# Performance work log

Hardware: AMD Instinct MI355X
Metric: run time of the kernel (lower is better)

The kernel has to match this reference:

```python
import jax, jax.numpy as jnp
import numpy as np

GAMMA = 0.9          # EMA momentum for prototype update
N_CLASSES = 201      # 200 classes + 1 background
K_PROTO = 5          # prototypes per class
FG_THRESH = 0.5      # pca_fg_threshold
SK_EPS = 0.05        # sinkhorn temperature (SwAV-style)
SK_ITERS = 3         # sinkhorn iterations
PCA_ITERS = 10       # niter of torch.pca_lowrank


def _l2norm(x, axis=-1):
    return x / jnp.maximum(jnp.linalg.norm(x, axis=axis, keepdims=True), 1e-12)


def _pca_first_component(X, key):
    # Randomized power iteration for the top left singular vector of the
    # centered data (mirrors torch.pca_lowrank(X, q=1, center=True, niter=10)).
    Xc = X - X.mean(0, keepdims=True)            # [N, D]
    G = Xc.T @ Xc                                # [D, D]
    v = jax.random.normal(key, (X.shape[1],), X.dtype)
    v = v / jnp.linalg.norm(v)
    def body(v, _):
        v = G @ v
        return v / jnp.maximum(jnp.linalg.norm(v), 1e-12), None
    v, _ = jax.lax.scan(body, v, None, length=PCA_ITERS)
    u = Xc @ v                                   # [N]
    return u / jnp.maximum(jnp.linalg.norm(u), 1e-12)


def _masked_sinkhorn(logits, mask):
    # logits: [C, BN, K], mask: [C, BN] bool (rows belonging to class c).
    # Vectorized equivalent of the per-class sinkhorn_knopp(L_c): returns a
    # row-stochastic assignment on the masked rows, balanced over the K cols.
    tiny = 1e-9
    m = mask[..., None].astype(logits.dtype)     # [C, BN, 1]
    Q = jnp.exp(logits / SK_EPS) * m
    n_c = jnp.maximum(mask.sum(-1).astype(logits.dtype), 1.0)[:, None, None]
    K = Q.shape[-1]
    Q = Q / jnp.maximum(Q.sum((-2, -1), keepdims=True), tiny)
    for _ in range(SK_ITERS):
        Q = Q / jnp.maximum(Q.sum(-2, keepdims=True), tiny) / K   # balance cols
        Q = Q * m
        Q = Q / jnp.maximum(Q.sum(-1, keepdims=True), tiny) / n_c # balance rows
        Q = Q * m
    return Q * n_c  # each masked row sums to 1


def setup_inputs() -> dict:
    key = jax.random.key(0)
    k1, k2, k3 = jax.random.split(key, 3)
    B, n_patches, dim = 32, 1024, 768
    patch_tokens = jax.random.normal(k1, (B, n_patches, dim), jnp.float32)
    prototypes = 0.02 * jax.random.normal(k2, (N_CLASSES, K_PROTO, dim), jnp.float32)
    labels = jax.random.randint(k3, (B,), 0, 200).astype(jnp.int64)
    return {"patch_tokens": patch_tokens, "prototypes": prototypes, "labels": labels}


def reference(patch_tokens, prototypes, labels):
    B, n_patches, D = patch_tokens.shape

    pt_norm = _l2norm(patch_tokens)              # [B, N, D]
    proto_norm = _l2norm(prototypes)             # [C, K, D]
    # B n_patches dim, C K dim -> B n_patches C K
    logits = jnp.einsum('bnd,ckd->bnck', pt_norm, proto_norm)

    # ---- get_pseudo_patch_labels (PCA foreground extraction) ----
    X = patch_tokens.reshape(-1, D)
    U = _pca_first_component(X, jax.random.key(1))
    U_scaled = (U - U.min()) / (U.max() - U.min())
    fg = (U_scaled < FG_THRESH).reshape(B, n_patches)
    patch_labels = jnp.where(fg, labels[:, None], N_CLASSES - 1)  # [B, N] int

    # ---- update_prototypes, vectorized over the 201-class python loop ----
    pl_flat = patch_labels.reshape(-1)                            # [B*N]
    L = jnp.transpose(logits.reshape(-1, N_CLASSES, K_PROTO), (1, 0, 2))  # [C, BN, K]
    class_ids = jnp.arange(N_CLASSES)
    mask = pl_flat[None, :] == class_ids[:, None]                 # [C, BN]
    Q = _masked_sinkhorn(L, mask)                                 # [C, BN, K]
    # P_c_new = L_c_assignment.T @ I_c, batched over classes
    P_new = jnp.einsum('cnk,nd->ckd', Q, pt_norm.reshape(-1, D))  # [C, K, D]
    present = (labels[None, :] == class_ids[:, None]).any(-1)     # 'c in labels'
    ema = GAMMA * prototypes + (1.0 - GAMMA) * P_new              # momentum_update
    new_prototypes = jnp.where(present[:, None, None], ema, prototypes)

    image_prototype_logits = logits.max(1)        # [B, C, K]
    class_logits = image_prototype_logits.sum(-1) # [B, C]
    return class_logits, image_prototype_logits, new_prototypes
```

## Files before the change

### kernel.cpp

```cpp
#include <hip/hip_runtime.h>
#include <stdint.h>
#include <stddef.h>

#define DEV static __device__ __forceinline__

typedef __attribute__((ext_vector_type(8))) short bf16x8;
typedef __attribute__((ext_vector_type(4))) float f32x4;
typedef __attribute__((ext_vector_type(4))) int i32x4;

DEV float bf2f(unsigned short u){ union{unsigned int i; float f;} v; v.i = ((unsigned int)u)<<16; return v.f; }
DEV unsigned short f2bf(float f){ union{float f; unsigned int i;} v; v.f=f; unsigned int i=v.i;
  return (unsigned short)((i + 0x7FFFu + ((i>>16)&1u)) >> 16); }
DEV unsigned int fenc(float x){ unsigned int i = __float_as_uint(x); return (i & 0x80000000u) ? ~i : (i | 0x80000000u); }
DEV float fdec(unsigned int e){ unsigned int i = (e & 0x80000000u) ? (e & 0x7FFFFFFFu) : ~e; return __uint_as_float(i); }

DEV float waveSum(float s){
  for (int m=32;m;m>>=1) s += __shfl_xor(s, m, 64);
  return s;
}

DEV float blockSum(float v, float* red){
  int t = threadIdx.x;
  red[t] = v; __syncthreads();
  for (int k=128;k>0;k>>=1){ if (t<k) red[t] += red[t+k]; __syncthreads(); }
  float r = red[0]; __syncthreads();
  return r;
}

DEV void gl16(const void* g, void* lds){
  __builtin_amdgcn_global_load_lds(
      (const __attribute__((address_space(1))) void*)g,
      (__attribute__((address_space(3))) void*)lds, 16, 0, 0);
}

DEV float erfinv_f(float x){
  float w = -log1pf(-__fmul_rn(x,x));
  float p;
  if (w < 5.0f){
    w = w - 2.5f;
    p = 2.81022636e-08f;
    p = 3.43273939e-07f + p*w;
    p = -3.5233877e-06f + p*w;
    p = -4.39150654e-06f + p*w;
    p = 0.00021858087f + p*w;
    p = -0.00125372503f + p*w;
    p = -0.00417768164f + p*w;
    p = 0.246640727f + p*w;
    p = 1.50140941f + p*w;
  } else {
    w = sqrtf(w) - 3.0f;
    p = -0.000200214257f;
    p = 0.000100950558f + p*w;
    p = 0.00134934322f + p*w;
    p = -0.00367342844f + p*w;
    p = 0.00573950773f + p*w;
    p = -0.0076224613f + p*w;
    p = 0.00943887047f + p*w;
    p = 1.00167406f + p*w;
    p = 2.83297682f + p*w;
  }
  return p*x;
}

#define BN_TOT 32768
#define DIM 768
#define NCLS 201
#define KP 5
#define CKPAD 1024
#define GSPLIT 32
#define PSPLIT 8


__global__ void k_setup(unsigned int* ipl_enc, int* cnt, int* cur, int* present,
                        unsigned int* minmax, float* meansum,
                        const int* __restrict__ raw, int* __restrict__ lab,
                        float* __restrict__ v,
                        const float* __restrict__ protos, unsigned short* __restrict__ protn){
  int i = blockIdx.x*256 + threadIdx.x;
  ipl_enc[i] = 0u;
  if (i < NCLS){ cnt[i]=0; cur[i]=0; present[i]=0; }
  if (i < DIM) meansum[i] = 0.f;
  if (i == 0){
    minmax[0]=0xFFFFFFFFu; minmax[1]=0u;
    bool is64 = true;
    for (int j=0;j<8;j++){
      int lo = raw[2*j], hi = raw[2*j+1];
      if (hi != 0 || lo < 0 || lo >= NCLS-1){ is64 = false; break; }
    }
    for (int j=0;j<32;j++) lab[j] = is64 ? raw[2*j] : raw[j];
  }
  if (i < DIM){
    unsigned int ks[3] = {0u, 1u, 0x1BD11BDBu};
    const int rot0[4] = {13,15,26,6};
    const int rot1[4] = {17,29,16,24};
    unsigned int x0 = 0u, x1 = (unsigned int)i;
    x0 += ks[0]; x1 += ks[1];
    #pragma unroll
    for (int g=0; g<5; g++){
      const int* rr = (g&1) ? rot1 : rot0;
      #pragma unroll
      for (int j=0;j<4;j++){
        x0 += x1;
        x1 = (x1 << rr[j]) | (x1 >> (32-rr[j]));
        x1 ^= x0;
      }
      x0 += ks[(g+1)%3];
      x1 += ks[(g+2)%3] + (unsigned int)(g+1);
    }
    unsigned int b = x0 ^ x1;
    const float lo = __uint_as_float(0xBF7FFFFFu);
    const float sq2 = __uint_as_float(0x3FB504F3u);
    float f = __uint_as_float((b>>9) | 0x3F800000u) - 1.0f;
    float uu = __fadd_rn(__fmul_rn(f, 2.0f), lo);
    uu = fmaxf(lo, uu);
    v[i] = sq2 * erfinv_f(uu);
  }
  int l = threadIdx.x & 63;
  #pragma unroll
  for (int rr=0; rr<2; rr++){
    int row = blockIdx.x*8 + (threadIdx.x>>6)*2 + rr;
    if (row >= NCLS*KP){
      for (int j=0;j<12;j++) protn[(size_t)row*DIM + l + j*64] = 0;
    } else {
      const float* p = protos + (size_t)row*DIM;
      float x[12]; float s = 0.f;
      for (int j=0;j<12;j++){ x[j] = p[l + j*64]; s += x[j]*x[j]; }
      s = waveSum(s);
      float inv = 1.0f / fmaxf(sqrtf(s), 1e-12f);
      for (int j=0;j<12;j++) protn[(size_t)row*DIM + l + j*64] = f2bf(x[j]*inv);
    }
  }
}

__global__ void k_trans(const float* __restrict__ X, signed char* __restrict__ q1T,
                        signed char* __restrict__ q2T, float* __restrict__ meansum){
  __shared__ float tile[64][65];
  __shared__ float colsum[4][64];
  int n0 = blockIdx.x*64, c0 = blockIdx.y*64;
  int t = threadIdx.x;
  float part = 0.f;
  for (int i=0;i<16;i++){
    int idx = t + i*256; int r = idx>>6, c = idx&63;
    float x = X[(size_t)(n0+r)*DIM + c0+c];
    tile[r][c] = x;
    part += x;
  }
  colsum[t>>6][t&63] = part;
  __syncthreads();
  for (int i=0;i<4;i++){
    int flat = t + i*256;
    int c = flat>>4;
    int ng = flat&15;
    unsigned int p1 = 0, p2 = 0;
    #pragma unroll
    for (int j=0;j<4;j++){
      float x = tile[ng*4+j][c];
      int q1 = (int)rintf(x*16.0f);
      q1 = max(-127, min(127, q1));
      float r2 = x - (float)q1*(1.0f/16.0f);
      int q2 = (int)rintf(r2*2048.0f);
      q2 = max(-127, min(127, q2));
      p1 |= ((unsigned int)(q1 & 0xff)) << (8*j);
      p2 |= ((unsigned int)(q2 & 0xff)) << (8*j);
    }
    size_t o = (size_t)(c0+c)*BN_TOT + n0 + ng*4;
    *(unsigned int*)&q1T[o] = p1;
    *(unsigned int*)&q2T[o] = p2;
  }
  if (t < 64){
    float s = colsum[0][t]+colsum[1][t]+colsum[2][t]+colsum[3][t];
    atomicAdd(&meansum[c0+t], s);
  }
}

__global__ void k_ptn(const float* __restrict__ X, unsigned short* __restrict__ ptn){
  int row = blockIdx.x*4 + (threadIdx.x>>6);
  int l = threadIdx.x & 63;
  const float4* xr = (const float4*)(X + (size_t)row*DIM);
  float4 x4[3]; float s = 0.f;
  #pragma unroll
  for (int j=0;j<3;j++){
    x4[j] = xr[l + j*64];
    s += x4[j].x*x4[j].x + x4[j].y*x4[j].y + x4[j].z*x4[j].z + x4[j].w*x4[j].w;
  }
  s = waveSum(s);
  float inv = 1.0f / fmaxf(sqrtf(s), 1e-12f);
  #pragma unroll
  for (int j=0;j<3;j++){
    ushort4 o;
    o.x = f2bf(x4[j].x*inv); o.y = f2bf(x4[j].y*inv);
    o.z = f2bf(x4[j].z*inv); o.w = f2bf(x4[j].w*inv);
    *(ushort4*)&ptn[(size_t)row*DIM + 4*(l + j*64)] = o;
  }
}

__global__ __launch_bounds__(256) void k_gemm_logits(const unsigned short* __restrict__ A,
                                                     const unsigned short* __restrict__ Bt,
                                                     unsigned int* __restrict__ ipl_enc){
  __shared__ __align__(16) unsigned short As[128*32];
  __shared__ __align__(16) unsigned short Bs[128*32];
  __shared__ float red[2][2][64];
  int flat = blockIdx.y*8 + blockIdx.x;
  int xcd = flat & 7, j = flat >> 3;
  int mb = xcd*32 + (j>>3);
  int nb = j & 7;
  int t = threadIdx.x;
  int w = t>>6, l = t&63;
  int wr = w>>1, wc = w&1;

  int gu = (l&3) ^ ((l>>2)&3) ^ (l>>4);
  size_t lane_off = (size_t)(l>>2)*DIM + (size_t)gu*8;
  size_t baseA = (size_t)(mb*128)*DIM;
  size_t baseB = (size_t)(nb*128)*DIM;

  int physc = (l>>4) ^ (l&3) ^ ((l>>2)&3);
  int rdA = (wr*64 + (l&15))*32 + physc*8;
  int rdB = (wc*64 + (l&15))*32 + physc*8;

  f32x4 acc[4][4];
  #pragma unroll
  for (int m=0;m<4;m++)
    #pragma unroll
    for (int n=0;n<4;n++){ acc[m][n][0]=0.f; acc[m][n][1]=0.f; acc[m][n][2]=0.f; acc[m][n][3]=0.f; }

  for (int kt=0; kt<24; kt++){
    size_t k0 = (size_t)kt*32;
    __syncthreads();
    #pragma unroll
    for (int ci=0; ci<2; ci++){
      int c = w + ci*4;
      size_t roff = (size_t)(c*16)*DIM + k0 + lane_off;
      gl16(A + baseA + roff, &As[c*512]);
      gl16(Bt + baseB + roff, &Bs[c*512]);
    }
    __syncthreads();
    bf16x8 a[4], b[4];
    #pragma unroll
    for (int m=0;m<4;m++) a[m] = *(const bf16x8*)&As[rdA + m*512];
    #pragma unroll
    for (int n=0;n<4;n++) b[n] = *(const bf16x8*)&Bs[rdB + n*512];
    #pragma unroll
    for (int m=0;m<4;m++)
      #pragma unroll
      for (int n=0;n<4;n++)
        acc[m][n] = __builtin_amdgcn_mfma_f32_16x16x32_bf16(a[m], b[n], acc[m][n], 0,0,0);
  }
  float vmax[4];
  #pragma unroll
  for (int n=0;n<4;n++){
    float v = -1e30f;
    #pragma unroll
    for (int m=0;m<4;m++)
      #pragma unroll
      for (int r=0;r<4;r++) v = fmaxf(v, acc[m][n][r]);
    v = fmaxf(v, __shfl_xor(v, 16, 64));
    v = fmaxf(v, __shfl_xor(v, 32, 64));
    vmax[n] = v;
  }
  __syncthreads();
  if (l < 16){
    #pragma unroll
    for (int n=0;n<4;n++) red[wc][wr][n*16 + l] = vmax[n];
  }
  __syncthreads();
  if (t < 128){
    int wcc = t>>6, col = t&63;
    float v = fmaxf(red[wcc][0][col], red[wcc][1][col]);
    int gcol = nb*128 + wcc*64 + col;
    if (gcol < NCLS*KP){
      int b = (mb*128) >> 10;
      atomicMax(&ipl_enc[b*CKPAD + gcol], fenc(v));
    }
  }
}

__global__ __launch_bounds__(256) void k_gemm_G(const signed char* __restrict__ q1T,
                                                const signed char* __restrict__ q2T,
                                                float* __restrict__ Gpart){
  __shared__ __align__(16) signed char A1[128*64];
  __shared__ __align__(16) signed char A2[128*64];
  __shared__ __align__(16) signed char B1[128*64];
  __shared__ __align__(16) signed char B2[128*64];
  int b = blockIdx.x;
  int xcd = b & 7, q = b >> 3;
  int s = xcd + 8*(q/21);
  int p = q % 21;
  int ib = 0, rem = p;
  while (rem >= 6 - ib){ rem -= 6 - ib; ib++; }
  int jb = ib + rem;
  int t = threadIdx.x, w = t>>6, l = t&63;
  int wr = w>>1, wc = w&1;

  int gu = (l&3) ^ ((l>>2)&3) ^ (l>>4);
  size_t lane_off = (size_t)(l>>2)*BN_TOT + (size_t)gu*16;
  size_t baseA = (size_t)(ib*128)*BN_TOT;
  size_t baseB = (size_t)(jb*128)*BN_TOT;

  int physc = (l>>4) ^ (l&3) ^ ((l>>2)&3);
  int rdA = (wr*64 + (l&15))*64 + physc*16;
  int rdB = (wc*64 + (l&15))*64 + physc*16;

  i32x4 acc1[4][4], acc2[4][4];
  #pragma unroll
  for (int m=0;m<4;m++)
    #pragma unroll
    for (int n=0;n<4;n++){
      acc1[m][n][0]=0; acc1[m][n][1]=0; acc1[m][n][2]=0; acc1[m][n][3]=0;
      acc2[m][n][0]=0; acc2[m][n][1]=0; acc2[m][n][2]=0; acc2[m][n][3]=0;
    }

  for (int kt=0; kt<16; kt++){
    size_t k0 = (size_t)s*1024 + (size_t)kt*64;
    __syncthreads();
    #pragma unroll
    for (int ci=0; ci<2; ci++){
      int c = w + ci*4;
      size_t roff = (size_t)(c*16)*BN_TOT + k0 + lane_off;
      gl16(q1T + baseA + roff, &A1[c*1024]);
      gl16(q2T + baseA + roff, &A2[c*1024]);
      gl16(q1T + baseB + roff, &B1[c*1024]);
      gl16(q2T + baseB + roff, &B2[c*1024]);
    }
    __syncthreads();
    i32x4 b1[4], b2[4];
    #pragma unroll
    for (int n=0;n<4;n++){
      b1[n] = *(const i32x4*)&B1[rdB + n*1024];
      b2[n] = *(const i32x4*)&B2[rdB + n*1024];
    }
    #pragma unroll
    for (int m=0;m<4;m++){
      i32x4 a1 = *(const i32x4*)&A1[rdA + m*1024];
      i32x4 a2 = *(const i32x4*)&A2[rdA + m*1024];
      #pragma unroll
      for (int n=0;n<4;n++){
        acc1[m][n] = __builtin_amdgcn_mfma_i32_16x16x64_i8(a1, b1[n], acc1[m][n], 0,0,0);
        acc2[m][n] = __builtin_amdgcn_mfma_i32_16x16x64_i8(a1, b2[n], acc2[m][n], 0,0,0);
        acc2[m][n] = __builtin_amdgcn_mfma_i32_16x16x64_i8(a2, b1[n], acc2[m][n], 0,0,0);
      }
    }
  }

  const float S11 = 1.0f/256.0f;
  const float S12 = 1.0f/32768.0f;
  float* out = Gpart + (size_t)s*DIM*DIM;
  #pragma unroll
  for (int m=0;m<4;m++)
    #pragma unroll
    for (int n=0;n<4;n++)
      #pragma unroll
      for (int r=0;r<4;r++){
        int row = ib*128 + wr*64 + m*16 + (l>>4)*4 + r;
        int col = jb*128 + wc*64 + n*16 + (l&15);
        float val = (float)acc1[m][n][r]*S11 + (float)acc2[m][n][r]*S12;
        out[(size_t)row*DIM + col] = val;
        if (ib != jb) out[(size_t)col*DIM + row] = val;
      }
}

__global__ void k_gfix(const float* __restrict__ Gpart, const float* __restrict__ meansum,
                       float* __restrict__ G){
  int i4 = blockIdx.x*256 + threadIdx.x;
  int i = i4*4;
  int r = i/DIM, c = i%DIM;
  float4 s = make_float4(0.f,0.f,0.f,0.f);
  for (int p=0;p<GSPLIT;p++){
    float4 g = *(const float4*)&Gpart[(size_t)p*DIM*DIM + i];
    s.x += g.x; s.y += g.y; s.z += g.z; s.w += g.w;
  }
  const float invN = 1.0f/32768.0f;
  float mr = meansum[r]*invN;
  float4 mc = *(const float4*)&meansum[c];
  float4 o;
  o.x = s.x*invN - mr*mc.x*invN;
  o.y = s.y*invN - mr*mc.y*invN;
  o.z = s.z*invN - mr*mc.z*invN;
  o.w = s.w*invN - mr*mc.w*invN;
  *(float4*)&G[i] = o;
}

__global__ void k_mv(const float* __restrict__ G, const float* __restrict__ vin,
                     float* __restrict__ vout){
  __shared__ float vs[DIM];
  int t = threadIdx.x;
  for (int i=t;i<DIM;i+=256) vs[i] = vin[i];
  __syncthreads();
  int row = blockIdx.x*4 + (t>>6), l = t&63;
  const float* g = G + (size_t)row*DIM;
  float s = 0.f;
  for (int j=0;j<12;j++) s += g[l + j*64]*vs[l + j*64];
  s = waveSum(s);
  if (l==0) vout[row] = s;
}

__global__ void k_u(const float* __restrict__ X, const float* __restrict__ v,
                    const float* __restrict__ meansum,
                    float* __restrict__ u, unsigned int* __restrict__ minmax){
  __shared__ float vs[DIM];
  __shared__ float red[256];
  __shared__ float smn[4], smx[4];
  int t = threadIdx.x;
  for (int i=t;i<DIM;i+=256) vs[i] = v[i];
  __syncthreads();
  float ps = 0.f;
  for (int i=t;i<DIM;i+=256) ps += meansum[i]*(1.0f/32768.0f)*vs[i];
  float scal = blockSum(ps, red);
  int w = t>>6, l = t&63;
  float mn = 1e30f, mx = -1e30f;
  #pragma unroll
  for (int rr=0; rr<4; rr++){
    int row = blockIdx.x*16 + w*4 + rr;
    const float4* xr = (const float4*)(X + (size_t)row*DIM);
    float s = 0.f;
    #pragma unroll
    for (int j=0;j<3;j++){
      float4 x4 = xr[l + j*64];
      int base = 4*(l + j*64);
      s += x4.x*vs[base] + x4.y*vs[base+1] + x4.z*vs[base+2] + x4.w*vs[base+3];
    }
    s = waveSum(s);
    if (l==0){
      float val = s - scal;
      u[row] = val;
      mn = fminf(mn, val); mx = fmaxf(mx, val);
    }
  }
  if (l==0){ smn[w]=mn; smx[w]=mx; }
  __syncthreads();
  if (t==0){
    for (int k=1;k<4;k++){ mn = fminf(mn, smn[k]); mx = fmaxf(mx, smx[k]); }
    atomicMin(&minmax[0], fenc(mn));
    atomicMax(&minmax[1], fenc(mx));
  }
}

__global__ void k_pl(const float* __restrict__ u, const int* __restrict__ labels,
                     const unsigned int* __restrict__ minmax, int* __restrict__ pl,
                     int* __restrict__ cnt){
  int n = blockIdx.x*256 + threadIdx.x;
  float umin = fdec(minmax[0]), umax = fdec(minmax[1]);
  float us = (u[n]-umin)/(umax-umin);
  int c = (us < 0.5f) ? labels[n>>10] : (NCLS-1);
  pl[n] = c;
  if (c < NCLS-1) atomicAdd(&cnt[c], 1);
}

__global__ void k_offs(const int* __restrict__ cnt, int* __restrict__ offs,
                       const int* __restrict__ labels, int* __restrict__ present){
  if (threadIdx.x == 0){
    int acc = 0;
    for (int c=0;c<NCLS-1;c++){ offs[c] = acc; acc += cnt[c]; }
    offs[NCLS-1] = acc;
  }
  if (threadIdx.x < 32) atomicOr(&present[labels[threadIdx.x]], 1);
}

__global__ void k_scatter(const int* __restrict__ pl, const int* __restrict__ offs,
                          int* __restrict__ cur, int* __restrict__ idx){
  int n = blockIdx.x*256 + threadIdx.x;
  int c = pl[n];
  if (c < NCLS-1){
    int p = offs[c] + atomicAdd(&cur[c], 1);
    idx[p] = n;
  }
}

__global__ void k_qlog(const int* __restrict__ idx, const int* __restrict__ offs,
                       const int* __restrict__ pl, const unsigned short* __restrict__ ptn,
                       const unsigned short* __restrict__ protn, float* __restrict__ q){
  int i = blockIdx.x*4 + (threadIdx.x>>6);
  int l = threadIdx.x & 63;
  int total = offs[NCLS-1];
  if (i >= total) return;
  int n = idx[i];
  int c = pl[n];
  const unsigned short* pr = ptn + (size_t)n*DIM;
  float x[12];
  for (int j=0;j<12;j++) x[j] = bf2f(pr[l + j*64]);
  for (int k=0;k<KP;k++){
    const unsigned short* wv = protn + (size_t)(c*KP + k)*DIM;
    float s = 0.f;
    for (int j=0;j<12;j++) s += x[j]*bf2f(wv[l + j*64]);
    s = waveSum(s);
    if (l==0) q[(size_t)i*KP + k] = expf(s*20.0f);
  }
}

__global__ void k_sink(const int* __restrict__ cnt, const int* __restrict__ offs,
                       float* __restrict__ q){
  __shared__ float red[256];
  __shared__ float colf[KP];
  int c = blockIdx.x;
  int nc = cnt[c];
  if (nc == 0) return;
  int n0 = offs[c];
  float* Q = q + (size_t)n0*KP;
  int t = threadIdx.x;
  int tot5 = nc*KP;
  float s = 0.f;
  for (int i=t;i<tot5;i+=256) s += Q[i];
  float total = blockSum(s, red);
  float sc = 1.0f/fmaxf(total, 1e-9f);
  for (int i=t;i<tot5;i+=256) Q[i] *= sc;
  __syncthreads();
  float ncf = (float)nc;
  for (int it=0; it<3; it++){
    float cs[KP] = {0,0,0,0,0};
    for (int i=t;i<nc;i+=256){
      const float* row = Q + (size_t)i*KP;
      #pragma unroll
      for (int k=0;k<KP;k++) cs[k] += row[k];
    }
    for (int k=0;k<KP;k++){
      float v = blockSum(cs[k], red);
      if (t==0) colf[k] = 1.0f/(fmaxf(v,1e-9f)*(float)KP);
    }
    __syncthreads();
    for (int i=t;i<nc;i+=256){
      float* row = Q + (size_t)i*KP;
      float qq[KP]; float rs = 0.f;
      #pragma unroll
      for (int k=0;k<KP;k++){ qq[k] = row[k]*colf[k]; rs += qq[k]; }
      float rf = 1.0f/(fmaxf(rs,1e-9f)*ncf);
      #pragma unroll
      for (int k=0;k<KP;k++) row[k] = qq[k]*rf;
    }
    __syncthreads();
  }
  for (int i=t;i<tot5;i+=256) Q[i] *= ncf;
}

__global__ void k_pnew(const int* __restrict__ cnt, const int* __restrict__ offs,
                       const int* __restrict__ present, const int* __restrict__ idx,
                       const float* __restrict__ q, const unsigned short* __restrict__ ptn,
                       float* __restrict__ P4){
  int c = blockIdx.y, s = blockIdx.x;
  if (!present[c]) return;
  int nc = cnt[c], n0 = offs[c];
  int r0 = n0 + (nc*s)/PSPLIT;
  int r1 = n0 + (nc*(s+1))/PSPLIT;
  int t = threadIdx.x;
  float acc[KP][3];
  #pragma unroll
  for (int k=0;k<KP;k++){ acc[k][0]=0.f; acc[k][1]=0.f; acc[k][2]=0.f; }
  for (int i=r0; i<r1; ++i){
    int n = idx[i];
    float qv[KP];
    #pragma unroll
    for (int k=0;k<KP;k++) qv[k] = q[(size_t)i*KP + k];
    const unsigned short* row = ptn + (size_t)n*DIM;
    #pragma unroll
    for (int j=0;j<3;j++){
      float x = bf2f(row[t + j*256]);
      #pragma unroll
      for (int k=0;k<KP;k++) acc[k][j] += qv[k]*x;
    }
  }
  float* out = P4 + ((size_t)(s*NCLS + c)*KP)*DIM;
  #pragma unroll
  for (int k=0;k<KP;k++)
    #pragma unroll
    for (int j=0;j<3;j++)
      out[(size_t)k*DIM + t + j*256] = acc[k][j];
}

__global__ void k_emafinal(const float* __restrict__ protos, const float* __restrict__ P4,
                           const int* __restrict__ present,
                           const unsigned int* __restrict__ ipl_enc,
                           float* __restrict__ out){
  int bid = blockIdx.x;
  if (bid < 3015){
    int i = bid*256 + threadIdx.x;
    if (i >= NCLS*KP*DIM) return;
    int c = i / (KP*DIM);
    float p = protos[i];
    float* o = out + 32*NCLS + 32*NCLS*KP;
    if (present[c]){
      float s = 0.f;
      #pragma unroll
      for (int sp=0; sp<PSPLIT; sp++) s += P4[(size_t)sp*NCLS*KP*DIM + i];
      o[i] = 0.9f*p + 0.1f*s;
    } else {
      o[i] = p;
    }
  } else {
    int i = (bid-3015)*256 + threadIdx.x;
    if (i < 32*NCLS*KP){
      int b = i / (NCLS*KP), ck = i % (NCLS*KP);
      out[32*NCLS + i] = fdec(ipl_enc[b*CKPAD + ck]);
    }
    if (i < 32*NCLS){
      int b = i / NCLS, c = i % NCLS;
      float s = 0.f;
      #pragma unroll
      for (int k=0;k<KP;k++) s += fdec(ipl_enc[b*CKPAD + c*KP + k]);
      out[b*NCLS + c] = s;
    }
  }
}

extern "C" void kernel_launch(void* const* d_in, const int* in_sizes, int n_in,
                              void* d_out, int out_size, void* d_ws, size_t ws_size,
                              hipStream_t stream){
  (void)in_sizes; (void)n_in; (void)out_size; (void)ws_size;
  const float* X = (const float*)d_in[0];
  const float* protos = (const float*)d_in[1];
  const int* labels_raw = (const int*)d_in[2];
  float* out = (float*)d_out;

  char* w = (char*)d_ws;
  size_t off = 0;
  auto alloc = [&](size_t bytes)->void*{
    void* p = (void*)(w + off);
    off = (off + bytes + 255) & ~(size_t)255;
    return p;
  };
  signed char* q1T      = (signed char*)alloc((size_t)DIM*BN_TOT);
  signed char* q2T      = (signed char*)alloc((size_t)DIM*BN_TOT);
  unsigned short* ptn   = (unsigned short*)alloc((size_t)BN_TOT*DIM*2);
  unsigned short* protn = (unsigned short*)alloc((size_t)CKPAD*DIM*2);
  float* Gpart   = (float*)alloc((size_t)GSPLIT*DIM*DIM*4);
  float* G       = (float*)alloc((size_t)DIM*DIM*4);
  float* meansum = (float*)alloc(DIM*4);
  float* vA      = (float*)alloc(DIM*4);
  float* vB      = (float*)alloc(DIM*4);
  int* cnt       = (int*)alloc(1024);
  int* cur       = (int*)alloc(1024);
  int* offs      = (int*)alloc(1024);
  int* present   = (int*)alloc(1024);
  int* labc      = (int*)alloc(256);
  unsigned int* minmax  = (unsigned int*)alloc(256);
  unsigned int* ipl_enc = (unsigned int*)alloc((size_t)32*CKPAD*4);

  char* gb = (char*)Gpart;
  size_t goff = 0;
  auto galloc = [&](size_t bytes)->void*{
    void* p = (void*)(gb + goff);
    goff = (goff + bytes + 255) & ~(size_t)255;
    return p;
  };
  float* u_  = (float*)galloc(BN_TOT*4);
  int* pl_   = (int*)galloc(BN_TOT*4);
  int* idx_  = (int*)galloc(BN_TOT*4);
  float* q_  = (float*)galloc((size_t)BN_TOT*KP*4);
  float* P4_ = (float*)galloc((size_t)PSPLIT*NCLS*KP*DIM*4);

  dim3 b256(256);
  k_setup<<<dim3(128), b256, 0, stream>>>(ipl_enc, cnt, cur, present, minmax, meansum,
                                          labels_raw, labc, vA, protos, protn);
  k_trans<<<dim3(512,12), b256, 0, stream>>>(X, q1T, q2T, meansum);
  k_ptn<<<dim3(8192), b256, 0, stream>>>(X, ptn);
  k_gemm_logits<<<dim3(8,256), b256, 0, stream>>>(ptn, protn, ipl_enc);
  k_gemm_G<<<dim3(21*GSPLIT), b256, 0, stream>>>(q1T, q2T, Gpart);
  k_gfix<<<dim3(576), b256, 0, stream>>>(Gpart, meansum, G);
  for (int it=0; it<10; it++){
    float* src = (it&1) ? vB : vA;
    float* dst = (it&1) ? vA : vB;
    k_mv<<<dim3(192), b256, 0, stream>>>(G, src, dst);
  }
  k_u<<<dim3(2048), b256, 0, stream>>>(X, vA, meansum, u_, minmax);
  k_pl<<<dim3(128), b256, 0, stream>>>(u_, labc, minmax, pl_, cnt);
  k_offs<<<dim3(1), b256, 0, stream>>>(cnt, offs, labc, present);
  k_scatter<<<dim3(128), b256, 0, stream>>>(pl_, offs, cur, idx_);
  k_qlog<<<dim3(8192), b256, 0, stream>>>(idx_, offs, pl_, ptn, protn, q_);
  k_sink<<<dim3(200), b256, 0, stream>>>(cnt, offs, q_);
  k_pnew<<<dim3(PSPLIT,NCLS), b256, 0, stream>>>(cnt, offs, present, idx_, q_, ptn, P4_);
  k_emafinal<<<dim3(3141), b256, 0, stream>>>(protos, P4_, present, ipl_enc, out);
}
```

Before: 483.0 us.

## Split int8 Gram GEMM into separate hi and cross-term kernels

```diff
diff --git a/kernel.cpp b/kernel.cpp
--- a/kernel.cpp
+++ b/kernel.cpp
@@ -67,6 +67,7 @@
 #define NCLS 201
 #define KP 5
 #define CKPAD 1024
+#define NSPLIT_G 16
 #define GSPLIT 32
 #define PSPLIT 8
 
@@ -274,20 +275,85 @@
   }
 }
 
-__global__ __launch_bounds__(256) void k_gemm_G(const signed char* __restrict__ q1T,
-                                                const signed char* __restrict__ q2T,
-                                                float* __restrict__ Gpart){
+DEV void g_coords(int b, int& s, int& ib, int& jb){
+  int xcd = b & 7, q = b >> 3;
+  s = xcd + 8*(q/21);
+  int p = q % 21;
+  ib = 0; int rem = p;
+  while (rem >= 6 - ib){ rem -= 6 - ib; ib++; }
+  jb = ib + rem;
+}
+
+__global__ __launch_bounds__(256) void k_gemm_G1(const signed char* __restrict__ q1T,
+                                                 float* __restrict__ Gpart){
+  __shared__ __align__(16) signed char A1[128*64];
+  __shared__ __align__(16) signed char B1[128*64];
+  int s, ib, jb; g_coords(blockIdx.x, s, ib, jb);
+  int t = threadIdx.x, w = t>>6, l = t&63;
+  int wr = w>>1, wc = w&1;
+
+  int gu = (l&3) ^ ((l>>2)&3) ^ (l>>4);
+  size_t lane_off = (size_t)(l>>2)*BN_TOT + (size_t)gu*16;
+  size_t baseA = (size_t)(ib*128)*BN_TOT;
+  size_t baseB = (size_t)(jb*128)*BN_TOT;
+
+  int physc = (l>>4) ^ (l&3) ^ ((l>>2)&3);
+  int rdA = (wr*64 + (l&15))*64 + physc*16;
+  int rdB = (wc*64 + (l&15))*64 + physc*16;
+
+  i32x4 acc[4][4];
+  #pragma unroll
+  for (int m=0;m<4;m++)
+    #pragma unroll
+    for (int n=0;n<4;n++){ acc[m][n][0]=0; acc[m][n][1]=0; acc[m][n][2]=0; acc[m][n][3]=0; }
+
+  for (int kt=0; kt<32; kt++){
+    size_t k0 = (size_t)s*2048 + (size_t)kt*64;
+    __syncthreads();
+    #pragma unroll
+    for (int ci=0; ci<2; ci++){
+      int c = w + ci*4;
+      size_t roff = (size_t)(c*16)*BN_TOT + k0 + lane_off;
+      gl16(q1T + baseA + roff, &A1[c*1024]);
+      gl16(q1T + baseB + roff, &B1[c*1024]);
+    }
+    __syncthreads();
+    i32x4 b1[4];
+    #pragma unroll
+    for (int n=0;n<4;n++) b1[n] = *(const i32x4*)&B1[rdB + n*1024];
+    #pragma unroll
+    for (int m=0;m<4;m++){
+      i32x4 a1 = *(const i32x4*)&A1[rdA + m*1024];
+      #pragma unroll
+      for (int n=0;n<4;n++)
+        acc[m][n] = __builtin_amdgcn_mfma_i32_16x16x64_i8(a1, b1[n], acc[m][n], 0,0,0);
+    }
+  }
+
+  const float S11 = 1.0f/256.0f;
+  float* out = Gpart + (size_t)s*DIM*DIM;
+  #pragma unroll
+  for (int m=0;m<4;m++)
+    #pragma unroll
+    for (int n=0;n<4;n++)
+      #pragma unroll
+      for (int r=0;r<4;r++){
+        int row = ib*128 + wr*64 + m*16 + (l>>4)*4 + r;
+        int col = jb*128 + wc*64 + n*16 + (l&15);
+        float val = (float)acc[m][n][r]*S11;
+        out[(size_t)row*DIM + col] = val;
+        if (ib != jb) out[(size_t)col*DIM + row] = val;
+      }
+}
+
+__global__ __launch_bounds__(256) void k_gemm_G2(const signed char* __restrict__ q1T,
+                                                 const signed char* __restrict__ q2T,
+                                                 float* __restrict__ Gpart2){
   __shared__ __align__(16) signed char A1[128*64];
   __shared__ __align__(16) signed char A2[128*64];
   __shared__ __align__(16) signed char B1[128*64];
   __shared__ __align__(16) signed char B2[128*64];
-  int b = blockIdx.x;
-  int xcd = b & 7, q = b >> 3;
-  int s = xcd + 8*(q/21);
-  int p = q % 21;
-  int ib = 0, rem = p;
-  while (rem >= 6 - ib){ rem -= 6 - ib; ib++; }
-  int jb = ib + rem;
+  int s, ib, jb; g_coords(blockIdx.x, s, ib, jb);
   int t = threadIdx.x, w = t>>6, l = t&63;
   int wr = w>>1, wc = w&1;
 
@@ -300,17 +366,14 @@
   int rdA = (wr*64 + (l&15))*64 + physc*16;
   int rdB = (wc*64 + (l&15))*64 + physc*16;
 
-  i32x4 acc1[4][4], acc2[4][4];
+  i32x4 acc[4][4];
   #pragma unroll
   for (int m=0;m<4;m++)
     #pragma unroll
-    for (int n=0;n<4;n++){
-      acc1[m][n][0]=0; acc1[m][n][1]=0; acc1[m][n][2]=0; acc1[m][n][3]=0;
-      acc2[m][n][0]=0; acc2[m][n][1]=0; acc2[m][n][2]=0; acc2[m][n][3]=0;
-    }
-
-  for (int kt=0; kt<16; kt++){
-    size_t k0 = (size_t)s*1024 + (size_t)kt*64;
+    for (int n=0;n<4;n++){ acc[m][n][0]=0; acc[m][n][1]=0; acc[m][n][2]=0; acc[m][n][3]=0; }
+
+  for (int kt=0; kt<32; kt++){
+    size_t k0 = (size_t)s*2048 + (size_t)kt*64;
     __syncthreads();
     #pragma unroll
     for (int ci=0; ci<2; ci++){
@@ -334,16 +397,14 @@
       i32x4 a2 = *(const i32x4*)&A2[rdA + m*1024];
       #pragma unroll
       for (int n=0;n<4;n++){
-        acc1[m][n] = __builtin_amdgcn_mfma_i32_16x16x64_i8(a1, b1[n], acc1[m][n], 0,0,0);
-        acc2[m][n] = __builtin_amdgcn_mfma_i32_16x16x64_i8(a1, b2[n], acc2[m][n], 0,0,0);
-        acc2[m][n] = __builtin_amdgcn_mfma_i32_16x16x64_i8(a2, b1[n], acc2[m][n], 0,0,0);
+        acc[m][n] = __builtin_amdgcn_mfma_i32_16x16x64_i8(a1, b2[n], acc[m][n], 0,0,0);
+        acc[m][n] = __builtin_amdgcn_mfma_i32_16x16x64_i8(a2, b1[n], acc[m][n], 0,0,0);
       }
     }
   }
 
-  const float S11 = 1.0f/256.0f;
   const float S12 = 1.0f/32768.0f;
-  float* out = Gpart + (size_t)s*DIM*DIM;
+  float* out = Gpart2 + (size_t)s*DIM*DIM;
   #pragma unroll
   for (int m=0;m<4;m++)
     #pragma unroll
@@ -352,7 +413,7 @@
       for (int r=0;r<4;r++){
         int row = ib*128 + wr*64 + m*16 + (l>>4)*4 + r;
         int col = jb*128 + wc*64 + n*16 + (l&15);
-        float val = (float)acc1[m][n][r]*S11 + (float)acc2[m][n][r]*S12;
+        float val = (float)acc[m][n][r]*S12;
         out[(size_t)row*DIM + col] = val;
         if (ib != jb) out[(size_t)col*DIM + row] = val;
       }
@@ -651,7 +712,8 @@
   k_trans<<<dim3(512,12), b256, 0, stream>>>(X, q1T, q2T, meansum);
   k_ptn<<<dim3(8192), b256, 0, stream>>>(X, ptn);
   k_gemm_logits<<<dim3(8,256), b256, 0, stream>>>(ptn, protn, ipl_enc);
-  k_gemm_G<<<dim3(21*GSPLIT), b256, 0, stream>>>(q1T, q2T, Gpart);
+  k_gemm_G1<<<dim3(21*NSPLIT_G), b256, 0, stream>>>(q1T, Gpart);
+  k_gemm_G2<<<dim3(21*NSPLIT_G), b256, 0, stream>>>(q1T, q2T, Gpart + (size_t)NSPLIT_G*DIM*DIM);
   k_gfix<<<dim3(576), b256, 0, stream>>>(Gpart, meansum, G);
   for (int it=0; it<10; it++){
     float* src = (it&1) ? vB : vA;
```

Result: no change. 489.9 us (+1.4%).

## Split int8 Gram GEMM into separate hi/cross chains and deepen K tiles

Applied to the files above, without the earlier changes.

```diff
diff --git a/kernel.cpp b/kernel.cpp
--- a/kernel.cpp
+++ b/kernel.cpp
@@ -67,6 +67,7 @@
 #define NCLS 201
 #define KP 5
 #define CKPAD 1024
+#define NSPLIT_G 16
 #define GSPLIT 32
 #define PSPLIT 8
 
@@ -197,8 +198,8 @@
 __global__ __launch_bounds__(256) void k_gemm_logits(const unsigned short* __restrict__ A,
                                                      const unsigned short* __restrict__ Bt,
                                                      unsigned int* __restrict__ ipl_enc){
-  __shared__ __align__(16) unsigned short As[128*32];
-  __shared__ __align__(16) unsigned short Bs[128*32];
+  __shared__ __align__(16) unsigned short As[128*64];
+  __shared__ __align__(16) unsigned short Bs[128*64];
   __shared__ float red[2][2][64];
   int flat = blockIdx.y*8 + blockIdx.x;
   int xcd = flat & 7, j = flat >> 3;
@@ -208,42 +209,42 @@
   int w = t>>6, l = t&63;
   int wr = w>>1, wc = w&1;
 
-  int gu = (l&3) ^ ((l>>2)&3) ^ (l>>4);
-  size_t lane_off = (size_t)(l>>2)*DIM + (size_t)gu*8;
+  int gu = (l&7) ^ ((l>>3)&7);
+  size_t lane_off = (size_t)(l>>3)*DIM + (size_t)gu*8;
   size_t baseA = (size_t)(mb*128)*DIM;
   size_t baseB = (size_t)(nb*128)*DIM;
 
-  int physc = (l>>4) ^ (l&3) ^ ((l>>2)&3);
-  int rdA = (wr*64 + (l&15))*32 + physc*8;
-  int rdB = (wc*64 + (l&15))*32 + physc*8;
-
   f32x4 acc[4][4];
   #pragma unroll
   for (int m=0;m<4;m++)
     #pragma unroll
     for (int n=0;n<4;n++){ acc[m][n][0]=0.f; acc[m][n][1]=0.f; acc[m][n][2]=0.f; acc[m][n][3]=0.f; }
 
-  for (int kt=0; kt<24; kt++){
-    size_t k0 = (size_t)kt*32;
+  for (int kt=0; kt<12; kt++){
+    size_t k0 = (size_t)kt*64;
     __syncthreads();
     #pragma unroll
-    for (int ci=0; ci<2; ci++){
-      int c = w + ci*4;
-      size_t roff = (size_t)(c*16)*DIM + k0 + lane_off;
-      gl16(A + baseA + roff, &As[c*512]);
-      gl16(Bt + baseB + roff, &Bs[c*512]);
+    for (int ci=0; ci<4; ci++){
+      int rg = w + ci*4;
+      size_t roff = (size_t)(rg*8)*DIM + k0 + lane_off;
+      gl16(A + baseA + roff, &As[rg*512]);
+      gl16(Bt + baseB + roff, &Bs[rg*512]);
     }
     __syncthreads();
-    bf16x8 a[4], b[4];
-    #pragma unroll
-    for (int m=0;m<4;m++) a[m] = *(const bf16x8*)&As[rdA + m*512];
-    #pragma unroll
-    for (int n=0;n<4;n++) b[n] = *(const bf16x8*)&Bs[rdB + n*512];
-    #pragma unroll
-    for (int m=0;m<4;m++)
-      #pragma unroll
-      for (int n=0;n<4;n++)
-        acc[m][n] = __builtin_amdgcn_mfma_f32_16x16x32_bf16(a[m], b[n], acc[m][n], 0,0,0);
+    #pragma unroll
+    for (int kk=0; kk<2; kk++){
+      int physb = (((kk*4) + (l>>4)) ^ (l&7))*8;
+      bf16x8 a[4], b[4];
+      #pragma unroll
+      for (int m=0;m<4;m++) a[m] = *(const bf16x8*)&As[(wr*64 + m*16 + (l&15))*64 + physb];
+      #pragma unroll
+      for (int n=0;n<4;n++) b[n] = *(const bf16x8*)&Bs[(wc*64 + n*16 + (l&15))*64 + physb];
+      #pragma unroll
+      for (int m=0;m<4;m++)
+        #pragma unroll
+        for (int n=0;n<4;n++)
+          acc[m][n] = __builtin_amdgcn_mfma_f32_16x16x32_bf16(a[m], b[n], acc[m][n], 0,0,0);
+    }
   }
   float vmax[4];
   #pragma unroll
@@ -274,76 +275,111 @@
   }
 }
 
-__global__ __launch_bounds__(256) void k_gemm_G(const signed char* __restrict__ q1T,
-                                                const signed char* __restrict__ q2T,
-                                                float* __restrict__ Gpart){
-  __shared__ __align__(16) signed char A1[128*64];
-  __shared__ __align__(16) signed char A2[128*64];
-  __shared__ __align__(16) signed char B1[128*64];
-  __shared__ __align__(16) signed char B2[128*64];
-  int b = blockIdx.x;
+DEV void g_coords(int b, int& s, int& ib, int& jb){
   int xcd = b & 7, q = b >> 3;
-  int s = xcd + 8*(q/21);
+  s = xcd + 8*(q/21);
   int p = q % 21;
-  int ib = 0, rem = p;
+  ib = 0; int rem = p;
   while (rem >= 6 - ib){ rem -= 6 - ib; ib++; }
-  int jb = ib + rem;
+  jb = ib + rem;
+}
+
+__global__ __launch_bounds__(256) void k_gemm_G12(const signed char* __restrict__ q1T,
+                                                  const signed char* __restrict__ q2T,
+                                                  float* __restrict__ Gpart){
+  __shared__ __align__(16) signed char LB[32768];
+  int bid = blockIdx.x;
+  int chain2 = (bid >= 21*NSPLIT_G);
+  int s, ib, jb; g_coords(chain2 ? bid - 21*NSPLIT_G : bid, s, ib, jb);
   int t = threadIdx.x, w = t>>6, l = t&63;
   int wr = w>>1, wc = w&1;
-
-  int gu = (l&3) ^ ((l>>2)&3) ^ (l>>4);
-  size_t lane_off = (size_t)(l>>2)*BN_TOT + (size_t)gu*16;
   size_t baseA = (size_t)(ib*128)*BN_TOT;
   size_t baseB = (size_t)(jb*128)*BN_TOT;
 
-  int physc = (l>>4) ^ (l&3) ^ ((l>>2)&3);
-  int rdA = (wr*64 + (l&15))*64 + physc*16;
-  int rdB = (wc*64 + (l&15))*64 + physc*16;
-
-  i32x4 acc1[4][4], acc2[4][4];
+  i32x4 acc[4][4];
   #pragma unroll
   for (int m=0;m<4;m++)
     #pragma unroll
-    for (int n=0;n<4;n++){
-      acc1[m][n][0]=0; acc1[m][n][1]=0; acc1[m][n][2]=0; acc1[m][n][3]=0;
-      acc2[m][n][0]=0; acc2[m][n][1]=0; acc2[m][n][2]=0; acc2[m][n][3]=0;
-    }
-
-  for (int kt=0; kt<16; kt++){
-    size_t k0 = (size_t)s*1024 + (size_t)kt*64;
-    __syncthreads();
-    #pragma unroll
-    for (int ci=0; ci<2; ci++){
-      int c = w + ci*4;
-      size_t roff = (size_t)(c*16)*BN_TOT + k0 + lane_off;
-      gl16(q1T + baseA + roff, &A1[c*1024]);
-      gl16(q2T + baseA + roff, &A2[c*1024]);
-      gl16(q1T + baseB + roff, &B1[c*1024]);
-      gl16(q2T + baseB + roff, &B2[c*1024]);
-    }
-    __syncthreads();
-    i32x4 b1[4], b2[4];
-    #pragma unroll
-    for (int n=0;n<4;n++){
-      b1[n] = *(const i32x4*)&B1[rdB + n*1024];
-      b2[n] = *(const i32x4*)&B2[rdB + n*1024];
-    }
-    #pragma unroll
-    for (int m=0;m<4;m++){
-      i32x4 a1 = *(const i32x4*)&A1[rdA + m*1024];
-      i32x4 a2 = *(const i32x4*)&A2[rdA + m*1024];
+    for (int n=0;n<4;n++){ acc[m][n][0]=0; acc[m][n][1]=0; acc[m][n][2]=0; acc[m][n][3]=0; }
+
+  float scale;
+  if (!chain2){
+    signed char* A1 = LB;
+    signed char* B1 = LB + 16384;
+    int gu = (l&7) ^ ((l>>3)&7);
+    size_t lane_off = (size_t)(l>>3)*BN_TOT + (size_t)gu*16;
+    for (int kt=0; kt<16; kt++){
+      size_t k0 = (size_t)s*2048 + (size_t)kt*128;
+      __syncthreads();
+      #pragma unroll
+      for (int ci=0; ci<4; ci++){
+        int rg = w + ci*4;
+        size_t roff = (size_t)(rg*8)*BN_TOT + k0 + lane_off;
+        gl16(q1T + baseA + roff, A1 + rg*1024);
+        gl16(q1T + baseB + roff, B1 + rg*1024);
+      }
+      __syncthreads();
+      #pragma unroll
+      for (int kk=0; kk<2; kk++){
+        int physb = (((kk*4) + (l>>4)) ^ (l&7))*16;
+        i32x4 b1[4];
+        #pragma unroll
+        for (int n=0;n<4;n++) b1[n] = *(const i32x4*)&B1[(wc*64 + n*16 + (l&15))*128 + physb];
+        #pragma unroll
+        for (int m=0;m<4;m++){
+          i32x4 a1 = *(const i32x4*)&A1[(wr*64 + m*16 + (l&15))*128 + physb];
+          #pragma unroll
+          for (int n=0;n<4;n++)
+            acc[m][n] = __builtin_amdgcn_mfma_i32_16x16x64_i8(a1, b1[n], acc[m][n], 0,0,0);
+        }
+      }
+    }
+    scale = 1.0f/256.0f;
+  } else {
+    signed char* A1 = LB;
+    signed char* A2 = LB + 8192;
+    signed char* B1 = LB + 16384;
+    signed char* B2 = LB + 24576;
+    int gu = (l&3) ^ ((l>>2)&3) ^ (l>>4);
+    size_t lane_off = (size_t)(l>>2)*BN_TOT + (size_t)gu*16;
+    int physc = (l>>4) ^ (l&3) ^ ((l>>2)&3);
+    int rdA = (wr*64 + (l&15))*64 + physc*16;
+    int rdB = (wc*64 + (l&15))*64 + physc*16;
+    for (int kt=0; kt<32; kt++){
+      size_t k0 = (size_t)s*2048 + (size_t)kt*64;
+      __syncthreads();
+      #pragma unroll
+      for (int ci=0; ci<2; ci++){
+        int c = w + ci*4;
+        size_t roff = (size_t)(c*16)*BN_TOT + k0 + lane_off;
+        gl16(q1T + baseA + roff, A1 + c*1024);
+        gl16(q2T + baseA + roff, A2 + c*1024);
+        gl16(q1T + baseB + roff, B1 + c*1024);
+        gl16(q2T + baseB + roff, B2 + c*1024);
+      }
+      __syncthreads();
+      i32x4 b1[4], b2[4];
       #pragma unroll
       for (int n=0;n<4;n++){
-        acc1[m][n] = __builtin_amdgcn_mfma_i32_16x16x64_i8(a1, b1[n], acc1[m][n], 0,0,0);
-        acc2[m][n] = __builtin_amdgcn_mfma_i32_16x16x64_i8(a1, b2[n], acc2[m][n], 0,0,0);
-        acc2[m][n] = __builtin_amdgcn_mfma_i32_16x16x64_i8(a2, b1[n], acc2[m][n], 0,0,0);
+        b1[n] = *(const i32x4*)&B1[rdB + n*1024];
+        b2[n] = *(const i32x4*)&B2[rdB + n*1024];
       }
-    }
-  }
-
-  const float S11 = 1.0f/256.0f;
-  const float S12 = 1.0f/32768.0f;
-  float* out = Gpart + (size_t)s*DIM*DIM;
+      #pragma unroll
+      for (int m=0;m<4;m++){
+        i32x4 a1 = *(const i32x4*)&A1[rdA + m*1024];
+        i32x4 a2 = *(const i32x4*)&A2[rdA + m*1024];
+        #pragma unroll
+        for (int n=0;n<4;n++){
+          acc[m][n] = __builtin_amdgcn_mfma_i32_16x16x64_i8(a1, b2[n], acc[m][n], 0,0,0);
+          acc[m][n] = __builtin_amdgcn_mfma_i32_16x16x64_i8(a2, b1[n], acc[m][n], 0,0,0);
+        }
+      }
+    }
+    scale = 1.0f/32768.0f;
+  }
+
+  int slice = chain2 ? (NSPLIT_G + s) : s;
+  float* out = Gpart + (size_t)slice*DIM*DIM;
   #pragma unroll
   for (int m=0;m<4;m++)
     #pragma unroll
@@ -352,7 +388,7 @@
       for (int r=0;r<4;r++){
         int row = ib*128 + wr*64 + m*16 + (l>>4)*4 + r;
         int col = jb*128 + wc*64 + n*16 + (l&15);
-        float val = (float)acc1[m][n][r]*S11 + (float)acc2[m][n][r]*S12;
+        float val = (float)acc[m][n][r]*scale;
         out[(size_t)row*DIM + col] = val;
         if (ib != jb) out[(size_t)col*DIM + row] = val;
       }
@@ -651,7 +687,7 @@
   k_trans<<<dim3(512,12), b256, 0, stream>>>(X, q1T, q2T, meansum);
   k_ptn<<<dim3(8192), b256, 0, stream>>>(X, ptn);
   k_gemm_logits<<<dim3(8,256), b256, 0, stream>>>(ptn, protn, ipl_enc);
-  k_gemm_G<<<dim3(21*GSPLIT), b256, 0, stream>>>(q1T, q2T, Gpart);
+  k_gemm_G12<<<dim3(2*21*NSPLIT_G), b256, 0, stream>>>(q1T, q2T, Gpart);
   k_gfix<<<dim3(576), b256, 0, stream>>>(Gpart, meansum, G);
   for (int it=0; it<10; it++){
     float* src = (it&1) ? vB : vA;
```

Result: faster. 458.4 us (-5.1%).
